# Performance work log

Measured on AMD Instinct MI355X. Metric: run time of the kernel, lower is better.

## Reference

```python
import jax, jax.numpy as jnp
from jax import lax
import numpy as np

B, T, I, H, OUT = 4096, 168, 4, 64, 12


def setup_inputs() -> dict:
    key = jax.random.key(0)
    ks = jax.random.split(key, 14)
    s = 0.05
    return {
        "x": jax.random.normal(ks[0], (B, T, I), dtype=jnp.float32),
        # LSTM layer 0 (PyTorch gate order: i, f, g, o)
        "Wih0": jax.random.normal(ks[1], (4 * H, I), dtype=jnp.float32) * s,
        "Whh0": jax.random.normal(ks[2], (4 * H, H), dtype=jnp.float32) * s,
        "bih0": jax.random.normal(ks[3], (4 * H,), dtype=jnp.float32) * s,
        "bhh0": jax.random.normal(ks[4], (4 * H,), dtype=jnp.float32) * s,
        # LSTM layer 1
        "Wih1": jax.random.normal(ks[5], (4 * H, H), dtype=jnp.float32) * s,
        "Whh1": jax.random.normal(ks[6], (4 * H, H), dtype=jnp.float32) * s,
        "bih1": jax.random.normal(ks[7], (4 * H,), dtype=jnp.float32) * s,
        "bhh1": jax.random.normal(ks[8], (4 * H,), dtype=jnp.float32) * s,
        # FC head: Linear(64,64) -> ReLU -> Linear(64,12)
        "W1": jax.random.normal(ks[9], (64, H), dtype=jnp.float32) * s,
        "b1": jax.random.normal(ks[10], (64,), dtype=jnp.float32) * s,
        "W2": jax.random.normal(ks[11], (OUT, 64), dtype=jnp.float32) * s,
        "b2": jax.random.normal(ks[12], (OUT,), dtype=jnp.float32) * s,
    }


def _lstm_layer(x, Wih, Whh, bih, bhh):
    # x: [B, T, in]; returns hidden sequence [B, T, H]
    Bsz = x.shape[0]
    Hd = Whh.shape[1]
    # Precompute input contribution for all timesteps: [B, T, 4H]
    xg = jnp.einsum('bti,gi->btg', x, Wih) + bih + bhh

    def step(carry, xg_t):
        h, c = carry
        g = xg_t + h @ Whh.T  # [B, 4H]
        i, f, gg, o = jnp.split(g, 4, axis=-1)
        i = jax.nn.sigmoid(i)
        f = jax.nn.sigmoid(f)
        gg = jnp.tanh(gg)
        o = jax.nn.sigmoid(o)
        c = f * c + i * gg
        h = o * jnp.tanh(c)
        return (h, c), h

    h0 = jnp.zeros((Bsz, Hd), x.dtype)
    (_, _), hs = lax.scan(step, (h0, h0), jnp.swapaxes(xg, 0, 1))  # hs: [T, B, H]
    return jnp.swapaxes(hs, 0, 1)


def reference(x, Wih0, Whh0, bih0, bhh0, Wih1, Whh1, bih1, bhh1, W1, b1, W2, b2):
    # Eval-mode forward: dropout layers are identity.
    h1 = _lstm_layer(x, Wih0, Whh0, bih0, bhh0)   # [B, T, H]
    h2 = _lstm_layer(h1, Wih1, Whh1, bih1, bhh1)  # [B, T, H]
    last = h2[:, -1, :]                            # [B, H]
    z = jax.nn.relu(last @ W1.T + b1)              # [B, 64]
    out = z @ W2.T + b2                            # [B, 12]
    return out.reshape(-1, 3, 4)
```

## Files before the change

kernel.cpp:

```cpp
#include <hip/hip_runtime.h>


typedef _Float16 h8 __attribute__((ext_vector_type(8)));
typedef _Float16 h4 __attribute__((ext_vector_type(4)));
typedef float f4 __attribute__((ext_vector_type(4)));

#define ROWB 208
#define HBUF (16 * ROWB)
#define XTAB_OFF 0
#define XTAB_BYTES (169 * 256)
#define H0_OFF XTAB_BYTES
#define H1_OFF (H0_OFF + 2 * HBUF)
#define SMEM_TOTAL (H1_OFF + 2 * HBUF)

#define K1F 1.4426950408889634f
#define K2F 2.8853900817779268f

__device__ __forceinline__ float exp2_(float x) {
#if __has_builtin(__builtin_amdgcn_exp2f)
  return __builtin_amdgcn_exp2f(x);
#else
  float r; asm("v_exp_f32 %0, %1" : "=v"(r) : "v"(x)); return r;
#endif
}
__device__ __forceinline__ float rcp_(float x) {
#if __has_builtin(__builtin_amdgcn_rcpf)
  return __builtin_amdgcn_rcpf(x);
#else
  float r; asm("v_rcp_f32 %0, %1" : "=v"(r) : "v"(x)); return r;
#endif
}

__device__ __forceinline__ f4 mfma16(h8 a, h8 b, f4 c) {
  return __builtin_amdgcn_mfma_f32_16x16x32_f16(a, b, c, 0, 0, 0);
}

__device__ __forceinline__ h8 load_w8s(const float* __restrict__ p, float sc) {
  h8 r;
#pragma unroll
  for (int j = 0; j < 8; j++) r[j] = (_Float16)(p[j] * sc);
  return r;
}

__device__ __forceinline__ void lstm_act(f4 a, float& c, float& h) {
  float Ei = exp2_(-a[0]);
  float Ef = exp2_(-a[1]);
  float Eg = exp2_(a[2]);
  float Eo = exp2_(-a[3]);
  float A = 1.f + Ei, B = 1.f + Ef, C = 1.f + Eg, D = 1.f + Eo;
  float AB = A * B, CD = C * D, BD = B * D;
  float R  = rcp_(AB * CD);
  float fv = (A * CD) * R;
  float ig = (BD * (Eg - 1.f)) * R;
  float ov = (AB * C) * R;
  c = fv * c + ig;
  float r2 = rcp_(exp2_(c * K2F) + 1.f);
  h = ov * (1.f - 2.f * r2);
}

extern "C" __global__ void __launch_bounds__(512, 2)
weather_lstm_mfma6(const float* __restrict__ x,
                   const float* __restrict__ Wih0, const float* __restrict__ Whh0,
                   const float* __restrict__ bih0, const float* __restrict__ bhh0,
                   const float* __restrict__ Wih1, const float* __restrict__ Whh1,
                   const float* __restrict__ bih1, const float* __restrict__ bhh1,
                   const float* __restrict__ W1, const float* __restrict__ b1,
                   const float* __restrict__ W2, const float* __restrict__ b2,
                   float* __restrict__ out)
{
  __shared__ __align__(16) unsigned char smem[SMEM_TOTAL];
  const int tid  = threadIdx.x;
  const int lane = tid & 63;
  const int w    = tid >> 6;
  const int col  = lane & 15;
  const int quad = lane >> 4;
  const int sB   = blockIdx.x * 16;

  const int g_  = col & 3;
  const int ul_ = col >> 2;
  const float asc = (g_ == 2) ? K2F : K1F;

  h8 a0[2][3], a1i[2][2], a1h[2][2];
#pragma unroll
  for (int t = 0; t < 2; t++) {
    const int r = g_ * 64 + w * 8 + t * 4 + ul_;
#pragma unroll
    for (int f = 0; f < 2; f++) {
      a0[t][f]  = load_w8s(Whh0 + r * 64 + f * 32 + quad * 8, asc);
      a1i[t][f] = load_w8s(Wih1 + r * 64 + f * 32 + quad * 8, asc);
      a1h[t][f] = load_w8s(Whh1 + r * 64 + f * 32 + quad * 8, asc);
    }
    h8 xw = {};
    if (quad == 0) {
#pragma unroll
      for (int j = 0; j < 4; j++) xw[j] = (_Float16)(Wih0[r * 4 + j] * asc);
    }
    a0[t][2] = xw;
  }

  f4 bias0v[2], bias1v[2];
#pragma unroll
  for (int t = 0; t < 2; t++) {
#pragma unroll
    for (int reg = 0; reg < 4; reg++) {
      const int rr = reg * 64 + w * 8 + t * 4 + quad;
      const float bs = (reg == 2) ? K2F : K1F;
      bias0v[t][reg] = (bih0[rr] + bhh0[rr]) * bs;
      bias1v[t][reg] = (bih1[rr] + bhh1[rr]) * bs;
    }
  }

  for (int idx = tid; idx < SMEM_TOTAL / 4; idx += 512) ((int*)smem)[idx] = 0;
  __syncthreads();
  for (int idx = tid; idx < 16 * 168; idx += 512) {
    const int c_ = idx / 168, t_ = idx - c_ * 168;
    f4 xv = *(const f4*)(x + ((size_t)(sB + c_) * 168 + t_) * 4);
    h4 xh;
#pragma unroll
    for (int j = 0; j < 4; j++) xh[j] = (_Float16)xv[j];
    *(h4*)(smem + XTAB_OFF + t_ * 256 + c_ * 16) = xh;
  }
  __syncthreads();

  float c0[2] = {0.f, 0.f}, c1[2] = {0.f, 0.f}, hl[2] = {0.f, 0.f};
  const int bo  = col * ROWB + quad * 16;
  const int wo0 = col * ROWB + (w * 8 + quad) * 2;
  const unsigned char* xp = smem + XTAB_OFF + col * 16;

  for (int k = 0; k <= 168; k++) {
    const int kb = k & 1, kbn = kb ^ 1;
    const unsigned char* h0r = smem + H0_OFF + kbn * HBUF;
    unsigned char*       h0w = smem + H0_OFF + kb  * HBUF;
    const unsigned char* h1r = smem + H1_OFF + kb  * HBUF;
    unsigned char*       h1w = smem + H1_OFF + kbn * HBUF;

    h8 b0  = *(const h8*)(h0r + bo);
    h8 b1v = *(const h8*)(h0r + bo + 64);
    h8 bx  = *(const h8*)(xp + k * 256);
    h8 q0  = *(const h8*)(h1r + bo);
    h8 q1  = *(const h8*)(h1r + bo + 64);

    f4 A[2], C[2];
#pragma unroll
    for (int t = 0; t < 2; t++) {
      A[t] = mfma16(a0[t][0], b0, bias0v[t]);
      C[t] = mfma16(a1i[t][0], b0, bias1v[t]);
      A[t] = mfma16(a0[t][1], b1v, A[t]);
      C[t] = mfma16(a1i[t][1], b1v, C[t]);
      A[t] = mfma16(a0[t][2], bx, A[t]);
      C[t] = mfma16(a1h[t][0], q0, C[t]);
      C[t] = mfma16(a1h[t][1], q1, C[t]);
    }

    if (k < 168) {
#pragma unroll
      for (int t = 0; t < 2; t++) {
        float h0o;
        lstm_act(A[t], c0[t], h0o);
        *(_Float16*)(h0w + wo0 + t * 8) = (_Float16)h0o;
      }
    }
    if (k > 0) {
#pragma unroll
      for (int t = 0; t < 2; t++) {
        lstm_act(C[t], c1[t], hl[t]);
        *(_Float16*)(h1w + wo0 + t * 8) = (_Float16)hl[t];
      }
    }
    __syncthreads();
  }

  float* fh = (float*)smem;
#pragma unroll
  for (int t = 0; t < 2; t++)
    fh[col * 64 + (w * 8 + t * 4 + quad)] = hl[t];
  __syncthreads();

  {
    const int u = tid & 63, grp = tid >> 6;
    const float* w1r = W1 + u * 64;
    float* zl = (float*)(smem + 4096);
#pragma unroll
    for (int rep = 0; rep < 2; rep++) {
      const int s = grp + rep * 8;
      float za = b1[u];
      const float* f0 = fh + s * 64;
      for (int j = 0; j < 64; j++) za += w1r[j] * f0[j];
      zl[s * 64 + u] = fmaxf(za, 0.f);
    }
  }
  __syncthreads();

  if (tid < 192) {
    const float* zl = (const float*)(smem + 4096);
    const int s = tid / 12, o = tid - s * 12;
    float a = b2[o];
    for (int j = 0; j < 64; j++) a += W2[o * 64 + j] * zl[s * 64 + j];
    out[(sB + s) * 12 + o] = a;
  }
}

extern "C" void kernel_launch(void* const* d_in, const int* in_sizes, int n_in,
                              void* d_out, int out_size, void* d_ws, size_t ws_size,
                              hipStream_t stream) {
  (void)in_sizes; (void)n_in; (void)d_ws; (void)ws_size; (void)out_size;
  const float* x    = (const float*)d_in[0];
  const float* Wih0 = (const float*)d_in[1];
  const float* Whh0 = (const float*)d_in[2];
  const float* bih0 = (const float*)d_in[3];
  const float* bhh0 = (const float*)d_in[4];
  const float* Wih1 = (const float*)d_in[5];
  const float* Whh1 = (const float*)d_in[6];
  const float* bih1 = (const float*)d_in[7];
  const float* bhh1 = (const float*)d_in[8];
  const float* W1   = (const float*)d_in[9];
  const float* b1   = (const float*)d_in[10];
  const float* W2   = (const float*)d_in[11];
  const float* b2   = (const float*)d_in[12];

  weather_lstm_mfma6<<<dim3(256), dim3(512), 0, stream>>>(
      x, Wih0, Whh0, bih0, bhh0, Wih1, Whh1, bih1, bhh1, W1, b1, W2, b2,
      (float*)d_out);
}
```

Baseline: 230.7 us.

## Stream x per step from global and stagger layer order across waves

Drops the LDS x table, which cut shared memory from about 69KB to about 13KB, and instead prefetches each timestep's x from global memory one step ahead in registers. Waves are split into two roles: half compute layer 0 first and then layer 1, the other half do the reverse. The aim is to interleave MFMA and transcendental work across waves on a SIMD so the matrix and vector units overlap. The trade-off is a global load on every step's critical path and more divergent code, though the smaller LDS footprint could allow more blocks per CU.

```diff
diff --git a/kernel.cpp b/kernel.cpp
--- a/kernel.cpp
+++ b/kernel.cpp
@@ -7,11 +7,9 @@
 
 #define ROWB 208
 #define HBUF (16 * ROWB)
-#define XTAB_OFF 0
-#define XTAB_BYTES (169 * 256)
-#define H0_OFF XTAB_BYTES
-#define H1_OFF (H0_OFF + 2 * HBUF)
-#define SMEM_TOTAL (H1_OFF + 2 * HBUF)
+#define H0_OFF 0
+#define H1_OFF (2 * HBUF)
+#define SMEM_TOTAL (4 * HBUF)
 
 #define K1F 1.4426950408889634f
 #define K2F 2.8853900817779268f
@@ -59,14 +57,14 @@
 }
 
 extern "C" __global__ void __launch_bounds__(512, 2)
-weather_lstm_mfma6(const float* __restrict__ x,
-                   const float* __restrict__ Wih0, const float* __restrict__ Whh0,
-                   const float* __restrict__ bih0, const float* __restrict__ bhh0,
-                   const float* __restrict__ Wih1, const float* __restrict__ Whh1,
-                   const float* __restrict__ bih1, const float* __restrict__ bhh1,
-                   const float* __restrict__ W1, const float* __restrict__ b1,
-                   const float* __restrict__ W2, const float* __restrict__ b2,
-                   float* __restrict__ out)
+weather_lstm_mfma14(const float* __restrict__ x,
+                    const float* __restrict__ Wih0, const float* __restrict__ Whh0,
+                    const float* __restrict__ bih0, const float* __restrict__ bhh0,
+                    const float* __restrict__ Wih1, const float* __restrict__ Whh1,
+                    const float* __restrict__ bih1, const float* __restrict__ bhh1,
+                    const float* __restrict__ W1, const float* __restrict__ b1,
+                    const float* __restrict__ W2, const float* __restrict__ b2,
+                    float* __restrict__ out)
 {
   __shared__ __align__(16) unsigned char smem[SMEM_TOTAL];
   const int tid  = threadIdx.x;
@@ -75,6 +73,7 @@
   const int col  = lane & 15;
   const int quad = lane >> 4;
   const int sB   = blockIdx.x * 16;
+  const int roleA = ((w ^ (w >> 2)) & 1) == 0;
 
   const int g_  = col & 3;
   const int ul_ = col >> 2;
@@ -112,20 +111,14 @@
 
   for (int idx = tid; idx < SMEM_TOTAL / 4; idx += 512) ((int*)smem)[idx] = 0;
   __syncthreads();
-  for (int idx = tid; idx < 16 * 168; idx += 512) {
-    const int c_ = idx / 168, t_ = idx - c_ * 168;
-    f4 xv = *(const f4*)(x + ((size_t)(sB + c_) * 168 + t_) * 4);
-    h4 xh;
-#pragma unroll
-    for (int j = 0; j < 4; j++) xh[j] = (_Float16)xv[j];
-    *(h4*)(smem + XTAB_OFF + t_ * 256 + c_ * 16) = xh;
-  }
-  __syncthreads();
+
+  f4 xc = {};
+  if (quad == 0)
+    xc = *(const f4*)(x + ((size_t)(sB + col) * 168 + 0) * 4);
 
   float c0[2] = {0.f, 0.f}, c1[2] = {0.f, 0.f}, hl[2] = {0.f, 0.f};
-  const int bo  = col * ROWB + quad * 16;
-  const int wo0 = col * ROWB + (w * 8 + quad) * 2;
-  const unsigned char* xp = smem + XTAB_OFF + col * 16;
+  const int bo = col * ROWB + quad * 16;
+  const int wo = col * ROWB + (w * 8 + quad) * 2;
 
   for (int k = 0; k <= 168; k++) {
     const int kb = k & 1, kbn = kb ^ 1;
@@ -134,37 +127,85 @@
     const unsigned char* h1r = smem + H1_OFF + kb  * HBUF;
     unsigned char*       h1w = smem + H1_OFF + kbn * HBUF;
 
-    h8 b0  = *(const h8*)(h0r + bo);
-    h8 b1v = *(const h8*)(h0r + bo + 64);
-    h8 bx  = *(const h8*)(xp + k * 256);
-    h8 q0  = *(const h8*)(h1r + bo);
-    h8 q1  = *(const h8*)(h1r + bo + 64);
+    h8 bx = {};
+    if (quad == 0) {
+#pragma unroll
+      for (int j = 0; j < 4; j++) bx[j] = (_Float16)xc[j];
+    }
+    {
+      const int kn = (k < 167) ? k + 1 : 167;
+      f4 xn = xc;
+      if (quad == 0)
+        xn = *(const f4*)(x + ((size_t)(sB + col) * 168 + kn) * 4);
+      xc = xn;
+    }
 
     f4 A[2], C[2];
-#pragma unroll
-    for (int t = 0; t < 2; t++) {
-      A[t] = mfma16(a0[t][0], b0, bias0v[t]);
-      C[t] = mfma16(a1i[t][0], b0, bias1v[t]);
-      A[t] = mfma16(a0[t][1], b1v, A[t]);
-      C[t] = mfma16(a1i[t][1], b1v, C[t]);
-      A[t] = mfma16(a0[t][2], bx, A[t]);
-      C[t] = mfma16(a1h[t][0], q0, C[t]);
-      C[t] = mfma16(a1h[t][1], q1, C[t]);
-    }
-
-    if (k < 168) {
-#pragma unroll
-      for (int t = 0; t < 2; t++) {
-        float h0o;
-        lstm_act(A[t], c0[t], h0o);
-        *(_Float16*)(h0w + wo0 + t * 8) = (_Float16)h0o;
-      }
-    }
-    if (k > 0) {
-#pragma unroll
-      for (int t = 0; t < 2; t++) {
-        lstm_act(C[t], c1[t], hl[t]);
-        *(_Float16*)(h1w + wo0 + t * 8) = (_Float16)hl[t];
+    if (roleA) {
+      h8 b0  = *(const h8*)(h0r + bo);
+      h8 b1v = *(const h8*)(h0r + bo + 64);
+#pragma unroll
+      for (int t = 0; t < 2; t++) {
+        A[t] = mfma16(a0[t][0], b0, bias0v[t]);
+        A[t] = mfma16(a0[t][1], b1v, A[t]);
+        A[t] = mfma16(a0[t][2], bx, A[t]);
+      }
+      if (k < 168) {
+#pragma unroll
+        for (int t = 0; t < 2; t++) {
+          float h0o;
+          lstm_act(A[t], c0[t], h0o);
+          *(_Float16*)(h0w + wo + t * 8) = (_Float16)h0o;
+        }
+      }
+      h8 q0 = *(const h8*)(h1r + bo);
+      h8 q1 = *(const h8*)(h1r + bo + 64);
+#pragma unroll
+      for (int t = 0; t < 2; t++) {
+        C[t] = mfma16(a1i[t][0], b0, bias1v[t]);
+        C[t] = mfma16(a1i[t][1], b1v, C[t]);
+        C[t] = mfma16(a1h[t][0], q0, C[t]);
+        C[t] = mfma16(a1h[t][1], q1, C[t]);
+      }
+      if (k > 0) {
+#pragma unroll
+        for (int t = 0; t < 2; t++) {
+          lstm_act(C[t], c1[t], hl[t]);
+          *(_Float16*)(h1w + wo + t * 8) = (_Float16)hl[t];
+        }
+      }
+    } else {
+      h8 b0  = *(const h8*)(h0r + bo);
+      h8 b1v = *(const h8*)(h0r + bo + 64);
+      h8 q0  = *(const h8*)(h1r + bo);
+      h8 q1  = *(const h8*)(h1r + bo + 64);
+#pragma unroll
+      for (int t = 0; t < 2; t++) {
+        C[t] = mfma16(a1i[t][0], b0, bias1v[t]);
+        C[t] = mfma16(a1i[t][1], b1v, C[t]);
+        C[t] = mfma16(a1h[t][0], q0, C[t]);
+        C[t] = mfma16(a1h[t][1], q1, C[t]);
+      }
+      if (k > 0) {
+#pragma unroll
+        for (int t = 0; t < 2; t++) {
+          lstm_act(C[t], c1[t], hl[t]);
+          *(_Float16*)(h1w + wo + t * 8) = (_Float16)hl[t];
+        }
+      }
+#pragma unroll
+      for (int t = 0; t < 2; t++) {
+        A[t] = mfma16(a0[t][0], b0, bias0v[t]);
+        A[t] = mfma16(a0[t][1], b1v, A[t]);
+        A[t] = mfma16(a0[t][2], bx, A[t]);
+      }
+      if (k < 168) {
+#pragma unroll
+        for (int t = 0; t < 2; t++) {
+          float h0o;
+          lstm_act(A[t], c0[t], h0o);
+          *(_Float16*)(h0w + wo + t * 8) = (_Float16)h0o;
+        }
       }
     }
     __syncthreads();
@@ -218,7 +259,7 @@
   const float* W2   = (const float*)d_in[11];
   const float* b2   = (const float*)d_in[12];
 
-  weather_lstm_mfma6<<<dim3(256), dim3(512), 0, stream>>>(
+  weather_lstm_mfma14<<<dim3(256), dim3(512), 0, stream>>>(
       x, Wih0, Whh0, bih0, bhh0, Wih1, Whh1, bih1, bhh1, W1, b1, W2, b2,
       (float*)d_out);
 }
```

Measured after the change: 252.0 us. 9.2% more time.
